# Performance work log

Measured on AMD Instinct MI355X. Metric: run time of the kernel, lower is better.

## Reference

```python
import jax, jax.numpy as jnp
import numpy as np

DM, H, B, SQ, SK = 512, 8, 8, 1024, 1024


def setup_inputs() -> dict:
    key = jax.random.key(0)
    ks = jax.random.split(key, 9)
    s = 0.02
    return {
        "Q": jax.random.normal(ks[0], (B, SQ, DM), jnp.float32),
        "K": jax.random.normal(ks[1], (B, SK, DM), jnp.float32),
        "V": jax.random.normal(ks[2], (B, SK, DM), jnp.float32),
        "mask": jax.random.randint(ks[3], (B, 1, SK), 0, 2, jnp.int32),
        "Wq": jax.random.normal(ks[4], (DM, DM), jnp.float32) * s,
        "bq": jnp.zeros((DM,), jnp.float32),
        "Wk": jax.random.normal(ks[5], (DM, DM), jnp.float32) * s,
        "bk": jnp.zeros((DM,), jnp.float32),
        "Wv": jax.random.normal(ks[6], (DM, DM), jnp.float32) * s,
        "bv": jnp.zeros((DM,), jnp.float32),
        "Wl": jax.random.normal(ks[7], (H * DM, DM), jnp.float32) * s,
        "bl": jnp.zeros((DM,), jnp.float32),
    }


def reference(Q, K, V, mask, Wq, bq, Wk, bk, Wv, bv, Wl, bl):
    # NB: the original loops h times with the SAME dense layers on full dm,
    # so all 'heads' are identical; compute once and replicate (same math).
    dm = Wq.shape[1]
    h = Wl.shape[0] // dm
    Ql = Q @ Wq + bq                                   # [B, Sq, dm]
    Kl = K @ Wk + bk                                   # [B, Sk, dm]
    Vl = V @ Wv + bv                                   # [B, Sk, dm]
    scale = jnp.sqrt(jnp.asarray(dm, jnp.float32))
    scores = jnp.einsum('bqd,bkd->bqk', Ql, Kl) / scale  # [B, Sq, Sk]
    scores = scores + mask.astype(scores.dtype) * (-1e9)  # mask [B,1,Sk] broadcasts
    att = jax.nn.softmax(scores, axis=-1)              # [B, Sq, Sk]
    head = jnp.einsum('bqk,bkd->bqd', att, Vl)         # [B, Sq, dm]
    multi = jnp.tile(head, (1, 1, h))                  # concat of h identical heads
    att_ws = jnp.broadcast_to(att[:, None], (att.shape[0], h) + att.shape[1:])
    Y = multi @ Wl + bl                                # [B, Sq, dm]
    return Y, att_ws
```

## Files before the change

kernel.cpp:

```cpp
#include <hip/hip_runtime.h>
#include <stdint.h>


typedef unsigned short u16;
typedef __attribute__((ext_vector_type(8))) short bf16x8;
typedef __attribute__((ext_vector_type(8))) unsigned short u16x8;
typedef __attribute__((ext_vector_type(4))) unsigned short u16x4;
typedef __attribute__((ext_vector_type(4))) float f32x4;

__device__ __forceinline__ u16 f2bf(float f) {
    union { float f; unsigned int u; } v; v.f = f;
    v.u += 0x7fffu + ((v.u >> 16) & 1u);
    return (u16)(v.u >> 16);
}
__device__ __forceinline__ float bf2f(u16 u) {
    union { unsigned int u; float f; } v; v.u = (unsigned int)u << 16;
    return v.f;
}

__device__ __forceinline__ void gld16(const u16* g, u16* l) {
#if __has_builtin(__builtin_amdgcn_global_load_lds)
    __builtin_amdgcn_global_load_lds(
        (const __attribute__((address_space(1))) void*)g,
        (__attribute__((address_space(3))) void*)l, 16, 0, 0);
#else
    *(uint4*)l = *(const uint4*)g;
#endif
}

__device__ __forceinline__ void gemm_core(
    const u16* __restrict__ Ab, const u16* __restrict__ Bb,
    int K, int lda, int ldb, int m0, int n0, int t,
    u16 (*As)[32], u16 (*Bs)[32], f32x4 acc[4][4])
{
    const int lane = t & 63;
    const int wm = ((t >> 6) & 1) * 64;
    const int wn = (t >> 7) * 64;
    const int sr = t >> 2, sc = (t & 3) * 8;
    const int fr = lane & 15, fk = (lane >> 4) * 8;

    for (int k0 = 0; k0 < K; k0 += 32) {
        const u16* ap = Ab + (long)(m0 + sr) * lda + (k0 + sc);
        const u16* bp = Bb + (long)(n0 + sr) * ldb + (k0 + sc);
        gld16(ap,             &As[sr][sc]);
        gld16(ap + 64L * lda, &As[sr + 64][sc]);
        gld16(bp,             &Bs[sr][sc]);
        gld16(bp + 64L * ldb, &Bs[sr + 64][sc]);
        __syncthreads();

        bf16x8 af[4], bfv[4];
        #pragma unroll
        for (int i = 0; i < 4; i++) af[i]  = *(const bf16x8*)&As[wm + i*16 + fr][fk];
        #pragma unroll
        for (int j = 0; j < 4; j++) bfv[j] = *(const bf16x8*)&Bs[wn + j*16 + fr][fk];
        #pragma unroll
        for (int i = 0; i < 4; i++)
            #pragma unroll
            for (int j = 0; j < 4; j++)
                acc[i][j] = __builtin_amdgcn_mfma_f32_16x16x32_bf16(af[i], bfv[j], acc[i][j], 0, 0, 0);
        __syncthreads();
    }
}

__device__ __forceinline__ void gemm_epilogue(
    int mode, void* Cv, const float* bias, const int* maskp,
    float scale, int ldc, int m0, int n0, int t, f32x4 acc[4][4])
{
    const int lane = t & 63;
    const int wm = ((t >> 6) & 1) * 64;
    const int wn = (t >> 7) * 64;
    const int cl = lane & 15, rl = (lane >> 4) * 4;

    float badd[4];
    #pragma unroll
    for (int j = 0; j < 4; j++) {
        int col = n0 + wn + j * 16 + cl;
        float v = bias ? bias[col] : 0.f;
        if (maskp) v += (float)maskp[col] * (-1e9f);
        badd[j] = v;
    }

    if (mode == 1) {
        u16* C = (u16*)Cv;
        #pragma unroll
        for (int i = 0; i < 4; i++)
            #pragma unroll
            for (int r = 0; r < 4; r++) {
                long row = m0 + wm + i * 16 + rl + r;
                #pragma unroll
                for (int j = 0; j < 4; j++)
                    C[(long)(n0 + wn + j * 16 + cl) * ldc + row] =
                        f2bf(acc[i][j][r] * scale + badd[j]);
            }
    } else if (mode == 2) {
        float* C = (float*)Cv;
        #pragma unroll
        for (int i = 0; i < 4; i++)
            #pragma unroll
            for (int r = 0; r < 4; r++) {
                float* crow = C + (long)(m0 + wm + i * 16 + rl + r) * ldc;
                #pragma unroll
                for (int j = 0; j < 4; j++)
                    crow[n0 + wn + j * 16 + cl] = acc[i][j][r] * scale + badd[j];
            }
    } else {
        u16* C = (u16*)Cv;
        #pragma unroll
        for (int i = 0; i < 4; i++)
            #pragma unroll
            for (int r = 0; r < 4; r++) {
                u16* crow = C + (long)(m0 + wm + i * 16 + rl + r) * ldc;
                #pragma unroll
                for (int j = 0; j < 4; j++)
                    crow[n0 + wn + j * 16 + cl] = f2bf(acc[i][j][r] * scale + badd[j]);
            }
    }
}

__global__ __launch_bounds__(256, 2)
void gemm_tn(const u16* __restrict__ A, const u16* __restrict__ B, void* __restrict__ Cv,
             const float* __restrict__ bias, const int* __restrict__ mask,
             int K, int lda, int ldb, int ldc,
             long sA, long sB, long sC, long sMask, float scale, int mode)
{
    __shared__ __align__(16) u16 As[128][32];
    __shared__ __align__(16) u16 Bs[128][32];
    const int bz = blockIdx.z;
    const int m0 = blockIdx.x * 128, n0 = blockIdx.y * 128;
    const int t = threadIdx.x;

    f32x4 acc[4][4];
    #pragma unroll
    for (int i = 0; i < 4; i++)
        #pragma unroll
        for (int j = 0; j < 4; j++) acc[i][j] = (f32x4){0.f, 0.f, 0.f, 0.f};

    gemm_core(A + (long)bz * sA, B + (long)bz * sB, K, lda, ldb, m0, n0, t, As, Bs, acc);

    void* Cb = (mode == 2) ? (void*)((float*)Cv + (long)bz * sC)
                           : (void*)((u16*)Cv + (long)bz * sC);
    const int* maskp = mask ? mask + (long)bz * sMask : nullptr;
    gemm_epilogue(mode, Cb, bias, maskp, scale, ldc, m0, n0, t, acc);
}

__global__ __launch_bounds__(256, 2)
void gemm_qkvv(const u16* __restrict__ Qb, const u16* __restrict__ Kb,
               const u16* __restrict__ Vb, const u16* __restrict__ Wqt,
               const u16* __restrict__ Wkt, const u16* __restrict__ Wct,
               u16* __restrict__ Qlb, u16* __restrict__ Klb, u16* __restrict__ Vwt,
               const float* __restrict__ bq, const float* __restrict__ bk,
               const float* __restrict__ bvs)
{
    __shared__ __align__(16) u16 As[128][32];
    __shared__ __align__(16) u16 Bs[128][32];
    const int z = blockIdx.z, seg = z >> 3, b = z & 7;
    const int m0 = blockIdx.x * 128, n0 = blockIdx.y * 128;
    const int t = threadIdx.x;
    const long sQ = 524288L;

    const u16* A; const u16* B; u16* C; const float* bias; int ldc, mode;
    if (seg == 0)      { A = Qb + b * sQ; B = Wqt; C = Qlb + b * sQ; bias = bq;  ldc = 512;  mode = 0; }
    else if (seg == 1) { A = Kb + b * sQ; B = Wkt; C = Klb + b * sQ; bias = bk;  ldc = 512;  mode = 0; }
    else               { A = Vb + b * sQ; B = Wct; C = Vwt + b * sQ; bias = bvs; ldc = 1024; mode = 1; }

    f32x4 acc[4][4];
    #pragma unroll
    for (int i = 0; i < 4; i++)
        #pragma unroll
        for (int j = 0; j < 4; j++) acc[i][j] = (f32x4){0.f, 0.f, 0.f, 0.f};

    gemm_core(A, B, 512, 512, 512, m0, n0, t, As, Bs, acc);
    gemm_epilogue(mode, C, bias, nullptr, 1.f, ldc, m0, n0, t, acc);
}

__global__ __launch_bounds__(256)
void prep_w(const float* __restrict__ Wq, const float* __restrict__ Wk,
            const float* __restrict__ Wv, const float* __restrict__ Wl,
            const float* __restrict__ bv,
            u16* __restrict__ Wqt, u16* __restrict__ Wkt,
            u16* __restrict__ Wvb, u16* __restrict__ Wst, float* __restrict__ bvs)
{
    const int bx = blockIdx.x;
    if (bx >= 4096) {
        int n = (bx - 4096) * 256 + threadIdx.x;
        if (n < 512) {
            float acc = 0.f;
            for (int k = 0; k < 512; k++) {
                float bvk = bv[k];
                if (bvk != 0.f) {
                    float s = 0.f;
                    #pragma unroll
                    for (int h = 0; h < 8; h++) s += Wl[((long)h * 512 + k) * 512 + n];
                    acc += bvk * s;
                }
            }
            bvs[n] = acc;
        }
        return;
    }
    long id = (long)bx * 256 + threadIdx.x;
    int seg = (int)(id >> 18);
    long j = id & 262143L;
    int n = (int)(j & 511), k = (int)(j >> 9);
    if (seg == 0) {
        Wqt[(long)n * 512 + k] = f2bf(Wq[(long)k * 512 + n]);
    } else if (seg == 1) {
        Wkt[(long)n * 512 + k] = f2bf(Wk[(long)k * 512 + n]);
    } else if (seg == 2) {
        Wvb[j] = f2bf(Wv[j]);
    } else {
        float s = 0.f;
        #pragma unroll
        for (int h = 0; h < 8; h++) s += Wl[((long)h * 512 + k) * 512 + n];
        Wst[(long)n * 512 + k] = f2bf(s);
    }
}

__global__ __launch_bounds__(256, 2)
void prep_qkv_wct(const float* __restrict__ Q, const float* __restrict__ K,
                  const float* __restrict__ V, u16* __restrict__ Qb,
                  u16* __restrict__ Kb, u16* __restrict__ Vb,
                  const u16* __restrict__ Wvb, const u16* __restrict__ Wst,
                  u16* __restrict__ Wct)
{
    __shared__ __align__(16) u16 As[128][32];
    __shared__ __align__(16) u16 Bs[128][32];
    const int bx = blockIdx.x;
    if (bx < 6144) {
        long id = (long)bx * 256 + threadIdx.x;
        int seg = (int)(id >> 19);
        long e = (id & 524287L) * 8;
        const float* s = seg == 0 ? Q : (seg == 1 ? K : V);
        u16* d = seg == 0 ? Qb : (seg == 1 ? Kb : Vb);
        float4 lo = *(const float4*)(s + e);
        float4 hi = *(const float4*)(s + e + 4);
        u16x8 r;
        r[0]=f2bf(lo.x); r[1]=f2bf(lo.y); r[2]=f2bf(lo.z); r[3]=f2bf(lo.w);
        r[4]=f2bf(hi.x); r[5]=f2bf(hi.y); r[6]=f2bf(hi.z); r[7]=f2bf(hi.w);
        *(u16x8*)(d + e) = r;
        return;
    }
    const int bid = bx - 6144;
    const int m0 = (bid & 3) * 128, n0 = (bid >> 2) * 128;
    const int t = threadIdx.x;
    f32x4 acc[4][4];
    #pragma unroll
    for (int i = 0; i < 4; i++)
        #pragma unroll
        for (int j = 0; j < 4; j++) acc[i][j] = (f32x4){0.f, 0.f, 0.f, 0.f};
    gemm_core(Wvb, Wst, 512, 512, 512, m0, n0, t, As, Bs, acc);
    gemm_epilogue(1, Wct, nullptr, nullptr, 1.f, 512, m0, n0, t, acc);
}

__global__ __launch_bounds__(256)
void softmax_rep(const u16* __restrict__ Sb, float* __restrict__ att,
                 u16* __restrict__ attb)
{
    const int q = blockIdx.x, b = blockIdx.y;
    const int t = threadIdx.x;
    const u16* row = Sb + ((long)b * 1024 + q) * 1024;

    u16x4 xv = *(const u16x4*)(row + t * 4);
    float x[4] = { bf2f(xv[0]), bf2f(xv[1]), bf2f(xv[2]), bf2f(xv[3]) };

    float m = fmaxf(fmaxf(x[0], x[1]), fmaxf(x[2], x[3]));
    #pragma unroll
    for (int o = 32; o > 0; o >>= 1) m = fmaxf(m, __shfl_xor(m, o));
    __shared__ float red[4];
    const int w = t >> 6;
    if ((t & 63) == 0) red[w] = m;
    __syncthreads();
    m = fmaxf(fmaxf(red[0], red[1]), fmaxf(red[2], red[3]));
    __syncthreads();

    float e[4], s = 0.f;
    #pragma unroll
    for (int i = 0; i < 4; i++) { e[i] = __expf(x[i] - m); s += e[i]; }
    #pragma unroll
    for (int o = 32; o > 0; o >>= 1) s += __shfl_xor(s, o);
    if ((t & 63) == 0) red[w] = s;
    __syncthreads();
    s = red[0] + red[1] + red[2] + red[3];
    float inv = 1.f / s;

    float a0 = e[0]*inv, a1 = e[1]*inv, a2 = e[2]*inv, a3 = e[3]*inv;
    float4 ov = make_float4(a0, a1, a2, a3);
    #pragma unroll
    for (int h = 0; h < 8; h++)
        *(float4*)(att + (((long)b * 8 + h) * 1024 + q) * 1024 + t * 4) = ov;
    u16x4 bo; bo[0]=f2bf(a0); bo[1]=f2bf(a1); bo[2]=f2bf(a2); bo[3]=f2bf(a3);
    *(u16x4*)(attb + ((long)b * 1024 + q) * 1024 + t * 4) = bo;
}

extern "C" void kernel_launch(void* const* d_in, const int* in_sizes, int n_in,
                              void* d_out, int out_size, void* d_ws, size_t ws_size,
                              hipStream_t stream)
{
    (void)in_sizes; (void)n_in; (void)out_size; (void)ws_size;

    const float* Q    = (const float*)d_in[0];
    const float* Kin  = (const float*)d_in[1];
    const float* V    = (const float*)d_in[2];
    const int*   mask = (const int*)d_in[3];
    const float* Wq   = (const float*)d_in[4];
    const float* bq   = (const float*)d_in[5];
    const float* Wk   = (const float*)d_in[6];
    const float* bk   = (const float*)d_in[7];
    const float* Wv   = (const float*)d_in[8];
    const float* bv   = (const float*)d_in[9];
    const float* Wl   = (const float*)d_in[10];
    const float* bl   = (const float*)d_in[11];

    float* out  = (float*)d_out;
    float* Yout = out;
    float* att  = out + 4194304L;

    u16*   w    = (u16*)d_ws;
    float* bvs  = (float*)w;
    u16*   Qb   = w + 1024;
    u16*   Kb   = Qb + 4194304L;
    u16*   Vb   = Kb + 4194304L;
    u16*   Wqt  = Vb + 4194304L;
    u16*   Wkt  = Wqt + 262144L;
    u16*   Wvb  = Wkt + 262144L;
    u16*   Wst  = Wvb + 262144L;
    u16*   Wct  = Wst + 262144L;
    u16*   Qlb  = Wct + 262144L;
    u16*   Klb  = Qlb + 4194304L;
    u16*   Vwt  = Klb + 4194304L;
    u16*   Sb   = Vwt + 4194304L;
    u16*   attb = Sb + 8388608L;

    const long sQ  = 524288L;
    const long sAt = 1048576L;
    const float isc = 0.04419417382415922f;

    prep_w<<<dim3(4098), dim3(256), 0, stream>>>(Wq, Wk, Wv, Wl, bv,
                                                 Wqt, Wkt, Wvb, Wst, bvs);

    prep_qkv_wct<<<dim3(6160), dim3(256), 0, stream>>>(Q, Kin, V, Qb, Kb, Vb,
                                                       Wvb, Wst, Wct);

    gemm_qkvv<<<dim3(8, 4, 24), dim3(256), 0, stream>>>(
        Qb, Kb, Vb, Wqt, Wkt, Wct, Qlb, Klb, Vwt, bq, bk, bvs);

    gemm_tn<<<dim3(8, 8, 8), dim3(256), 0, stream>>>(
        Qlb, Klb, Sb, nullptr, mask, 512, 512, 512, 1024,
        sQ, sQ, sAt, 1024L, isc, 0);

    softmax_rep<<<dim3(1024, 8), dim3(256), 0, stream>>>(Sb, att, attb);

    gemm_tn<<<dim3(8, 4, 8), dim3(256), 0, stream>>>(
        attb, Vwt, Yout, bl, nullptr, 1024, 1024, 1024, 512,
        sAt, sQ, sQ, 0L, 1.f, 2);
}
```

Measured before the change: 469.5 us.

## Fuse QK^T, masked softmax, and PV GEMM into single attention kernel

Replaces the score GEMM, standalone softmax and output GEMM with one kernel. Each block handles 16 query rows over the full 1024-key range, keeping scores in registers and the bf16 probabilities in LDS for the PV product. This removes the bf16 score and probability round-trips through global memory and two kernel launches. In exchange, K and V operands are read directly from global memory without LDS tiling, with heavy redundant reloading across only 512 blocks. Register pressure is also high.

```diff
diff --git a/kernel.cpp b/kernel.cpp
--- a/kernel.cpp
+++ b/kernel.cpp
@@ -12,10 +12,6 @@
     union { float f; unsigned int u; } v; v.f = f;
     v.u += 0x7fffu + ((v.u >> 16) & 1u);
     return (u16)(v.u >> 16);
-}
-__device__ __forceinline__ float bf2f(u16 u) {
-    union { unsigned int u; float f; } v; v.u = (unsigned int)u << 16;
-    return v.f;
 }
 
 __device__ __forceinline__ void gld16(const u16* g, u16* l) {
@@ -63,7 +59,7 @@
 }
 
 __device__ __forceinline__ void gemm_epilogue(
-    int mode, void* Cv, const float* bias, const int* maskp,
+    int mode, void* Cv, const float* bias,
     float scale, int ldc, int m0, int n0, int t, f32x4 acc[4][4])
 {
     const int lane = t & 63;
@@ -75,9 +71,7 @@
     #pragma unroll
     for (int j = 0; j < 4; j++) {
         int col = n0 + wn + j * 16 + cl;
-        float v = bias ? bias[col] : 0.f;
-        if (maskp) v += (float)maskp[col] * (-1e9f);
-        badd[j] = v;
+        badd[j] = bias ? bias[col] : 0.f;
     }
 
     if (mode == 1) {
@@ -92,17 +86,6 @@
                     C[(long)(n0 + wn + j * 16 + cl) * ldc + row] =
                         f2bf(acc[i][j][r] * scale + badd[j]);
             }
-    } else if (mode == 2) {
-        float* C = (float*)Cv;
-        #pragma unroll
-        for (int i = 0; i < 4; i++)
-            #pragma unroll
-            for (int r = 0; r < 4; r++) {
-                float* crow = C + (long)(m0 + wm + i * 16 + rl + r) * ldc;
-                #pragma unroll
-                for (int j = 0; j < 4; j++)
-                    crow[n0 + wn + j * 16 + cl] = acc[i][j][r] * scale + badd[j];
-            }
     } else {
         u16* C = (u16*)Cv;
         #pragma unroll
@@ -118,32 +101,6 @@
 }
 
 __global__ __launch_bounds__(256, 2)
-void gemm_tn(const u16* __restrict__ A, const u16* __restrict__ B, void* __restrict__ Cv,
-             const float* __restrict__ bias, const int* __restrict__ mask,
-             int K, int lda, int ldb, int ldc,
-             long sA, long sB, long sC, long sMask, float scale, int mode)
-{
-    __shared__ __align__(16) u16 As[128][32];
-    __shared__ __align__(16) u16 Bs[128][32];
-    const int bz = blockIdx.z;
-    const int m0 = blockIdx.x * 128, n0 = blockIdx.y * 128;
-    const int t = threadIdx.x;
-
-    f32x4 acc[4][4];
-    #pragma unroll
-    for (int i = 0; i < 4; i++)
-        #pragma unroll
-        for (int j = 0; j < 4; j++) acc[i][j] = (f32x4){0.f, 0.f, 0.f, 0.f};
-
-    gemm_core(A + (long)bz * sA, B + (long)bz * sB, K, lda, ldb, m0, n0, t, As, Bs, acc);
-
-    void* Cb = (mode == 2) ? (void*)((float*)Cv + (long)bz * sC)
-                           : (void*)((u16*)Cv + (long)bz * sC);
-    const int* maskp = mask ? mask + (long)bz * sMask : nullptr;
-    gemm_epilogue(mode, Cb, bias, maskp, scale, ldc, m0, n0, t, acc);
-}
-
-__global__ __launch_bounds__(256, 2)
 void gemm_qkvv(const u16* __restrict__ Qb, const u16* __restrict__ Kb,
                const u16* __restrict__ Vb, const u16* __restrict__ Wqt,
                const u16* __restrict__ Wkt, const u16* __restrict__ Wct,
@@ -170,7 +127,7 @@
         for (int j = 0; j < 4; j++) acc[i][j] = (f32x4){0.f, 0.f, 0.f, 0.f};
 
     gemm_core(A, B, 512, 512, 512, m0, n0, t, As, Bs, acc);
-    gemm_epilogue(mode, C, bias, nullptr, 1.f, ldc, m0, n0, t, acc);
+    gemm_epilogue(mode, C, bias, 1.f, ldc, m0, n0, t, acc);
 }
 
 __global__ __launch_bounds__(256)
@@ -249,47 +206,150 @@
         #pragma unroll
         for (int j = 0; j < 4; j++) acc[i][j] = (f32x4){0.f, 0.f, 0.f, 0.f};
     gemm_core(Wvb, Wst, 512, 512, 512, m0, n0, t, As, Bs, acc);
-    gemm_epilogue(1, Wct, nullptr, nullptr, 1.f, 512, m0, n0, t, acc);
-}
-
-__global__ __launch_bounds__(256)
-void softmax_rep(const u16* __restrict__ Sb, float* __restrict__ att,
-                 u16* __restrict__ attb)
-{
-    const int q = blockIdx.x, b = blockIdx.y;
-    const int t = threadIdx.x;
-    const u16* row = Sb + ((long)b * 1024 + q) * 1024;
-
-    u16x4 xv = *(const u16x4*)(row + t * 4);
-    float x[4] = { bf2f(xv[0]), bf2f(xv[1]), bf2f(xv[2]), bf2f(xv[3]) };
-
-    float m = fmaxf(fmaxf(x[0], x[1]), fmaxf(x[2], x[3]));
-    #pragma unroll
-    for (int o = 32; o > 0; o >>= 1) m = fmaxf(m, __shfl_xor(m, o));
-    __shared__ float red[4];
-    const int w = t >> 6;
-    if ((t & 63) == 0) red[w] = m;
+    gemm_epilogue(1, Wct, nullptr, 1.f, 512, m0, n0, t, acc);
+}
+
+__global__ __launch_bounds__(256, 2)
+void fused_attn(const u16* __restrict__ Qlb, const u16* __restrict__ Klb,
+                const u16* __restrict__ Vwt, const int* __restrict__ mask,
+                const float* __restrict__ bl,
+                float* __restrict__ att, float* __restrict__ Yout)
+{
+    __shared__ u16 S[16][1032];
+    __shared__ float redm[4][16];
+    __shared__ float reds[4][16];
+
+    const int r0 = blockIdx.x * 16;
+    const int b  = blockIdx.y;
+    const int t  = threadIdx.x;
+    const int w  = t >> 6, lane = t & 63;
+    const int cl = lane & 15, q4 = lane >> 4;
+    const int rl = q4 * 4;
+    const int wkv = w * 256;
+    const int wn  = w * 128;
+    const float isc = 0.04419417382415922f;
+
+    const u16* Qb = Qlb + (long)b * 524288;
+    const u16* Kb = Klb + (long)b * 524288;
+    const u16* Vb = Vwt + (long)b * 524288;
+
+    bf16x8 af[16];
+    #pragma unroll
+    for (int ks = 0; ks < 16; ks++)
+        af[ks] = *(const bf16x8*)(Qb + (long)(r0 + cl) * 512 + ks * 32 + q4 * 8);
+
+    float mf[16];
+    #pragma unroll
+    for (int j = 0; j < 16; j++)
+        mf[j] = (float)mask[b * 1024 + wkv + j * 16 + cl] * (-1e9f);
+
+    f32x4 acc[16];
+    #pragma unroll
+    for (int j = 0; j < 16; j++) acc[j] = (f32x4){0.f, 0.f, 0.f, 0.f};
+
+    #pragma unroll
+    for (int ks = 0; ks < 16; ks++) {
+        #pragma unroll
+        for (int j = 0; j < 16; j++) {
+            bf16x8 bf = *(const bf16x8*)(Kb + (long)(wkv + j * 16 + cl) * 512 + ks * 32 + q4 * 8);
+            acc[j] = __builtin_amdgcn_mfma_f32_16x16x32_bf16(af[ks], bf, acc[j], 0, 0, 0);
+        }
+    }
+
+    #pragma unroll
+    for (int j = 0; j < 16; j++)
+        #pragma unroll
+        for (int r = 0; r < 4; r++)
+            acc[j][r] = acc[j][r] * isc + mf[j];
+
+    float m[4];
+    #pragma unroll
+    for (int r = 0; r < 4; r++) {
+        float v = acc[0][r];
+        #pragma unroll
+        for (int j = 1; j < 16; j++) v = fmaxf(v, acc[j][r]);
+        #pragma unroll
+        for (int o = 1; o < 16; o <<= 1) v = fmaxf(v, __shfl_xor(v, o));
+        m[r] = v;
+    }
+    if (cl == 0) {
+        #pragma unroll
+        for (int r = 0; r < 4; r++) redm[w][rl + r] = m[r];
+    }
     __syncthreads();
-    m = fmaxf(fmaxf(red[0], red[1]), fmaxf(red[2], red[3]));
+    #pragma unroll
+    for (int r = 0; r < 4; r++)
+        m[r] = fmaxf(fmaxf(redm[0][rl + r], redm[1][rl + r]),
+                     fmaxf(redm[2][rl + r], redm[3][rl + r]));
+
+    float sm[4] = {0.f, 0.f, 0.f, 0.f};
+    #pragma unroll
+    for (int j = 0; j < 16; j++)
+        #pragma unroll
+        for (int r = 0; r < 4; r++) {
+            float e = __expf(acc[j][r] - m[r]);
+            acc[j][r] = e;
+            sm[r] += e;
+        }
+    #pragma unroll
+    for (int r = 0; r < 4; r++)
+        #pragma unroll
+        for (int o = 1; o < 16; o <<= 1) sm[r] += __shfl_xor(sm[r], o);
+    if (cl == 0) {
+        #pragma unroll
+        for (int r = 0; r < 4; r++) reds[w][rl + r] = sm[r];
+    }
     __syncthreads();
-
-    float e[4], s = 0.f;
-    #pragma unroll
-    for (int i = 0; i < 4; i++) { e[i] = __expf(x[i] - m); s += e[i]; }
-    #pragma unroll
-    for (int o = 32; o > 0; o >>= 1) s += __shfl_xor(s, o);
-    if ((t & 63) == 0) red[w] = s;
+    float inv[4];
+    #pragma unroll
+    for (int r = 0; r < 4; r++)
+        inv[r] = 1.f / (reds[0][rl + r] + reds[1][rl + r] + reds[2][rl + r] + reds[3][rl + r]);
+
+    #pragma unroll
+    for (int j = 0; j < 16; j++)
+        #pragma unroll
+        for (int r = 0; r < 4; r++) {
+            float a = acc[j][r] * inv[r];
+            acc[j][r] = a;
+            S[rl + r][wkv + j * 16 + cl] = f2bf(a);
+        }
     __syncthreads();
-    s = red[0] + red[1] + red[2] + red[3];
-    float inv = 1.f / s;
-
-    float a0 = e[0]*inv, a1 = e[1]*inv, a2 = e[2]*inv, a3 = e[3]*inv;
-    float4 ov = make_float4(a0, a1, a2, a3);
-    #pragma unroll
-    for (int h = 0; h < 8; h++)
-        *(float4*)(att + (((long)b * 8 + h) * 1024 + q) * 1024 + t * 4) = ov;
-    u16x4 bo; bo[0]=f2bf(a0); bo[1]=f2bf(a1); bo[2]=f2bf(a2); bo[3]=f2bf(a3);
-    *(u16x4*)(attb + ((long)b * 1024 + q) * 1024 + t * 4) = bo;
+
+    #pragma unroll
+    for (int r = 0; r < 4; r++) {
+        long base_r = (((long)b * 8) * 1024 + (r0 + rl + r)) * 1024 + wkv + cl;
+        #pragma unroll
+        for (int h = 0; h < 8; h++) {
+            float* p = att + base_r + (long)h * 1048576;
+            #pragma unroll
+            for (int j = 0; j < 16; j++) p[j * 16] = acc[j][r];
+        }
+    }
+
+    f32x4 acc2[8];
+    #pragma unroll
+    for (int j = 0; j < 8; j++) acc2[j] = (f32x4){0.f, 0.f, 0.f, 0.f};
+
+    #pragma unroll
+    for (int ks = 0; ks < 32; ks++) {
+        bf16x8 afv = *(const bf16x8*)&S[cl][ks * 32 + q4 * 8];
+        #pragma unroll
+        for (int j = 0; j < 8; j++) {
+            bf16x8 bf = *(const bf16x8*)(Vb + (long)(wn + j * 16 + cl) * 1024 + ks * 32 + q4 * 8);
+            acc2[j] = __builtin_amdgcn_mfma_f32_16x16x32_bf16(afv, bf, acc2[j], 0, 0, 0);
+        }
+    }
+
+    float blv[8];
+    #pragma unroll
+    for (int j = 0; j < 8; j++) blv[j] = bl[wn + j * 16 + cl];
+    #pragma unroll
+    for (int r = 0; r < 4; r++) {
+        float* yrow = Yout + (long)b * 524288 + (long)(r0 + rl + r) * 512;
+        #pragma unroll
+        for (int j = 0; j < 8; j++)
+            yrow[wn + j * 16 + cl] = acc2[j][r] + blv[j];
+    }
 }
 
 extern "C" void kernel_launch(void* const* d_in, const int* in_sizes, int n_in,
@@ -328,12 +388,6 @@
     u16*   Qlb  = Wct + 262144L;
     u16*   Klb  = Qlb + 4194304L;
     u16*   Vwt  = Klb + 4194304L;
-    u16*   Sb   = Vwt + 4194304L;
-    u16*   attb = Sb + 8388608L;
-
-    const long sQ  = 524288L;
-    const long sAt = 1048576L;
-    const float isc = 0.04419417382415922f;
 
     prep_w<<<dim3(4098), dim3(256), 0, stream>>>(Wq, Wk, Wv, Wl, bv,
                                                  Wqt, Wkt, Wvb, Wst, bvs);
@@ -344,13 +398,6 @@
     gemm_qkvv<<<dim3(8, 4, 24), dim3(256), 0, stream>>>(
         Qb, Kb, Vb, Wqt, Wkt, Wct, Qlb, Klb, Vwt, bq, bk, bvs);
 
-    gemm_tn<<<dim3(8, 8, 8), dim3(256), 0, stream>>>(
-        Qlb, Klb, Sb, nullptr, mask, 512, 512, 512, 1024,
-        sQ, sQ, sAt, 1024L, isc, 0);
-
-    softmax_rep<<<dim3(1024, 8), dim3(256), 0, stream>>>(Sb, att, attb);
-
-    gemm_tn<<<dim3(8, 4, 8), dim3(256), 0, stream>>>(
-        attb, Vwt, Yout, bl, nullptr, 1024, 1024, 1024, 512,
-        sAt, sQ, sQ, 0L, 1.f, 2);
-}
+    fused_attn<<<dim3(64, 8), dim3(256), 0, stream>>>(
+        Qlb, Klb, Vwt, mask, bl, att, Yout);
+}
```

Measured after the change: 578.8 us. 23.3% more time.

## Fold Wq·Wkᵀ into one weight to drop the K projection GEMM

Applied to the files above, without the earlier changes.

Scores are rewritten as Q(WqWkᵀ)Kᵀ plus rank-one bias terms. A precomputed Wqk product is applied to Q only, and raw K feeds the score GEMM directly. Per-row u and per-column v bias vectors are added in the score epilogue. This removes one of the three batched projection GEMMs at the cost of a small weight GEMM and two matrix-vector passes, and it may change bf16 rounding behaviour.

```diff
diff --git a/kernel.cpp b/kernel.cpp
--- a/kernel.cpp
+++ b/kernel.cpp
@@ -64,6 +64,7 @@
 
 __device__ __forceinline__ void gemm_epilogue(
     int mode, void* Cv, const float* bias, const int* maskp,
+    const float* urow, const float* vcol,
     float scale, int ldc, int m0, int n0, int t, f32x4 acc[4][4])
 {
     const int lane = t & 63;
@@ -77,6 +78,7 @@
         int col = n0 + wn + j * 16 + cl;
         float v = bias ? bias[col] : 0.f;
         if (maskp) v += (float)maskp[col] * (-1e9f);
+        if (vcol)  v += vcol[col];
         badd[j] = v;
     }
 
@@ -87,10 +89,11 @@
             #pragma unroll
             for (int r = 0; r < 4; r++) {
                 long row = m0 + wm + i * 16 + rl + r;
+                float ua = urow ? urow[row] : 0.f;
                 #pragma unroll
                 for (int j = 0; j < 4; j++)
                     C[(long)(n0 + wn + j * 16 + cl) * ldc + row] =
-                        f2bf(acc[i][j][r] * scale + badd[j]);
+                        f2bf(acc[i][j][r] * scale + badd[j] + ua);
             }
     } else if (mode == 2) {
         float* C = (float*)Cv;
@@ -98,10 +101,12 @@
         for (int i = 0; i < 4; i++)
             #pragma unroll
             for (int r = 0; r < 4; r++) {
-                float* crow = C + (long)(m0 + wm + i * 16 + rl + r) * ldc;
+                int row = m0 + wm + i * 16 + rl + r;
+                float ua = urow ? urow[row] : 0.f;
+                float* crow = C + (long)row * ldc;
                 #pragma unroll
                 for (int j = 0; j < 4; j++)
-                    crow[n0 + wn + j * 16 + cl] = acc[i][j][r] * scale + badd[j];
+                    crow[n0 + wn + j * 16 + cl] = acc[i][j][r] * scale + badd[j] + ua;
             }
     } else {
         u16* C = (u16*)Cv;
@@ -109,10 +114,12 @@
         for (int i = 0; i < 4; i++)
             #pragma unroll
             for (int r = 0; r < 4; r++) {
-                u16* crow = C + (long)(m0 + wm + i * 16 + rl + r) * ldc;
+                int row = m0 + wm + i * 16 + rl + r;
+                float ua = urow ? urow[row] : 0.f;
+                u16* crow = C + (long)row * ldc;
                 #pragma unroll
                 for (int j = 0; j < 4; j++)
-                    crow[n0 + wn + j * 16 + cl] = f2bf(acc[i][j][r] * scale + badd[j]);
+                    crow[n0 + wn + j * 16 + cl] = f2bf(acc[i][j][r] * scale + badd[j] + ua);
             }
     }
 }
@@ -120,6 +127,7 @@
 __global__ __launch_bounds__(256, 2)
 void gemm_tn(const u16* __restrict__ A, const u16* __restrict__ B, void* __restrict__ Cv,
              const float* __restrict__ bias, const int* __restrict__ mask,
+             const float* __restrict__ u, const float* __restrict__ v,
              int K, int lda, int ldb, int ldc,
              long sA, long sB, long sC, long sMask, float scale, int mode)
 {
@@ -140,16 +148,16 @@
     void* Cb = (mode == 2) ? (void*)((float*)Cv + (long)bz * sC)
                            : (void*)((u16*)Cv + (long)bz * sC);
     const int* maskp = mask ? mask + (long)bz * sMask : nullptr;
-    gemm_epilogue(mode, Cb, bias, maskp, scale, ldc, m0, n0, t, acc);
+    const float* up = u ? u + (long)bz * 1024 : nullptr;
+    const float* vp = v ? v + (long)bz * 1024 : nullptr;
+    gemm_epilogue(mode, Cb, bias, maskp, up, vp, scale, ldc, m0, n0, t, acc);
 }
 
 __global__ __launch_bounds__(256, 2)
-void gemm_qkvv(const u16* __restrict__ Qb, const u16* __restrict__ Kb,
-               const u16* __restrict__ Vb, const u16* __restrict__ Wqt,
-               const u16* __restrict__ Wkt, const u16* __restrict__ Wct,
-               u16* __restrict__ Qlb, u16* __restrict__ Klb, u16* __restrict__ Vwt,
-               const float* __restrict__ bq, const float* __restrict__ bk,
-               const float* __restrict__ bvs)
+void gemm_tv(const u16* __restrict__ Qb, const u16* __restrict__ Vb,
+             const u16* __restrict__ Wqkt, const u16* __restrict__ Wct,
+             u16* __restrict__ T1b, u16* __restrict__ Vwt,
+             const float* __restrict__ bvs)
 {
     __shared__ __align__(16) u16 As[128][32];
     __shared__ __align__(16) u16 Bs[128][32];
@@ -158,57 +166,74 @@
     const int t = threadIdx.x;
     const long sQ = 524288L;
 
-    const u16* A; const u16* B; u16* C; const float* bias; int ldc, mode;
-    if (seg == 0)      { A = Qb + b * sQ; B = Wqt; C = Qlb + b * sQ; bias = bq;  ldc = 512;  mode = 0; }
-    else if (seg == 1) { A = Kb + b * sQ; B = Wkt; C = Klb + b * sQ; bias = bk;  ldc = 512;  mode = 0; }
-    else               { A = Vb + b * sQ; B = Wct; C = Vwt + b * sQ; bias = bvs; ldc = 1024; mode = 1; }
-
     f32x4 acc[4][4];
     #pragma unroll
     for (int i = 0; i < 4; i++)
         #pragma unroll
         for (int j = 0; j < 4; j++) acc[i][j] = (f32x4){0.f, 0.f, 0.f, 0.f};
 
-    gemm_core(A, B, 512, 512, 512, m0, n0, t, As, Bs, acc);
-    gemm_epilogue(mode, C, bias, nullptr, 1.f, ldc, m0, n0, t, acc);
+    if (seg == 0) {
+        gemm_core(Qb + b * sQ, Wqkt, 512, 512, 512, m0, n0, t, As, Bs, acc);
+        gemm_epilogue(0, T1b + b * sQ, nullptr, nullptr, nullptr, nullptr,
+                      1.f, 512, m0, n0, t, acc);
+    } else {
+        gemm_core(Vb + b * sQ, Wct, 512, 512, 512, m0, n0, t, As, Bs, acc);
+        gemm_epilogue(1, Vwt + b * sQ, bvs, nullptr, nullptr, nullptr,
+                      1.f, 1024, m0, n0, t, acc);
+    }
 }
 
 __global__ __launch_bounds__(256)
 void prep_w(const float* __restrict__ Wq, const float* __restrict__ Wk,
             const float* __restrict__ Wv, const float* __restrict__ Wl,
+            const float* __restrict__ bq, const float* __restrict__ bk,
             const float* __restrict__ bv,
-            u16* __restrict__ Wqt, u16* __restrict__ Wkt,
-            u16* __restrict__ Wvb, u16* __restrict__ Wst, float* __restrict__ bvs)
+            u16* __restrict__ Wqb, u16* __restrict__ Wkb,
+            u16* __restrict__ Wvb, u16* __restrict__ Wst,
+            float* __restrict__ bvs, float* __restrict__ wqbk,
+            float* __restrict__ wkbq, float* __restrict__ c0)
 {
     const int bx = blockIdx.x;
+    const int t  = threadIdx.x;
+    if (bx >= 4098) {
+        int i = (bx - 4098) * 256 + t;
+        float sq = 0.f, sk = 0.f;
+        for (int o = 0; o < 512; o++) {
+            sq += Wq[(long)i * 512 + o] * bk[o];
+            sk += Wk[(long)i * 512 + o] * bq[o];
+        }
+        wqbk[i] = sq;
+        wkbq[i] = sk;
+        if (bx == 4098 && t == 0) {
+            float s = 0.f;
+            for (int o = 0; o < 512; o++) s += bq[o] * bk[o];
+            c0[0] = s;
+        }
+        return;
+    }
     if (bx >= 4096) {
-        int n = (bx - 4096) * 256 + threadIdx.x;
-        if (n < 512) {
-            float acc = 0.f;
-            for (int k = 0; k < 512; k++) {
-                float bvk = bv[k];
-                if (bvk != 0.f) {
-                    float s = 0.f;
-                    #pragma unroll
-                    for (int h = 0; h < 8; h++) s += Wl[((long)h * 512 + k) * 512 + n];
-                    acc += bvk * s;
-                }
+        int n = (bx - 4096) * 256 + t;
+        float acc = 0.f;
+        for (int k = 0; k < 512; k++) {
+            float bvk = bv[k];
+            if (bvk != 0.f) {
+                float s = 0.f;
+                #pragma unroll
+                for (int h = 0; h < 8; h++) s += Wl[((long)h * 512 + k) * 512 + n];
+                acc += bvk * s;
             }
-            bvs[n] = acc;
-        }
+        }
+        bvs[n] = acc;
         return;
     }
-    long id = (long)bx * 256 + threadIdx.x;
+    long id = (long)bx * 256 + t;
     int seg = (int)(id >> 18);
     long j = id & 262143L;
-    int n = (int)(j & 511), k = (int)(j >> 9);
-    if (seg == 0) {
-        Wqt[(long)n * 512 + k] = f2bf(Wq[(long)k * 512 + n]);
-    } else if (seg == 1) {
-        Wkt[(long)n * 512 + k] = f2bf(Wk[(long)k * 512 + n]);
-    } else if (seg == 2) {
-        Wvb[j] = f2bf(Wv[j]);
-    } else {
+    if (seg == 0)      Wqb[j] = f2bf(Wq[j]);
+    else if (seg == 1) Wkb[j] = f2bf(Wk[j]);
+    else if (seg == 2) Wvb[j] = f2bf(Wv[j]);
+    else {
+        int n = (int)(j & 511), k = (int)(j >> 9);
         float s = 0.f;
         #pragma unroll
         for (int h = 0; h < 8; h++) s += Wl[((long)h * 512 + k) * 512 + n];
@@ -220,14 +245,20 @@
 void prep_qkv_wct(const float* __restrict__ Q, const float* __restrict__ K,
                   const float* __restrict__ V, u16* __restrict__ Qb,
                   u16* __restrict__ Kb, u16* __restrict__ Vb,
+                  const u16* __restrict__ Wqb, const u16* __restrict__ Wkb,
                   const u16* __restrict__ Wvb, const u16* __restrict__ Wst,
-                  u16* __restrict__ Wct)
+                  u16* __restrict__ Wqkt, u16* __restrict__ Wct,
+                  const float* __restrict__ wqbk, const float* __restrict__ wkbq,
+                  const float* __restrict__ c0,
+                  float* __restrict__ u, float* __restrict__ v)
 {
     __shared__ __align__(16) u16 As[128][32];
     __shared__ __align__(16) u16 Bs[128][32];
     const int bx = blockIdx.x;
+    const int t  = threadIdx.x;
+
     if (bx < 6144) {
-        long id = (long)bx * 256 + threadIdx.x;
+        long id = (long)bx * 256 + t;
         int seg = (int)(id >> 19);
         long e = (id & 524287L) * 8;
         const float* s = seg == 0 ? Q : (seg == 1 ? K : V);
@@ -240,16 +271,59 @@
         *(u16x8*)(d + e) = r;
         return;
     }
-    const int bid = bx - 6144;
-    const int m0 = (bid & 3) * 128, n0 = (bid >> 2) * 128;
-    const int t = threadIdx.x;
-    f32x4 acc[4][4];
-    #pragma unroll
-    for (int i = 0; i < 4; i++)
-        #pragma unroll
-        for (int j = 0; j < 4; j++) acc[i][j] = (f32x4){0.f, 0.f, 0.f, 0.f};
-    gemm_core(Wvb, Wst, 512, 512, 512, m0, n0, t, As, Bs, acc);
-    gemm_epilogue(1, Wct, nullptr, nullptr, 1.f, 512, m0, n0, t, acc);
+    if (bx < 6176) {
+        const int bid = bx - 6144;
+        const int which = bid >> 4;
+        const int sub = bid & 15;
+        const int m0 = (sub & 3) * 128, n0 = (sub >> 2) * 128;
+        f32x4 acc[4][4];
+        #pragma unroll
+        for (int i = 0; i < 4; i++)
+            #pragma unroll
+            for (int j = 0; j < 4; j++) acc[i][j] = (f32x4){0.f, 0.f, 0.f, 0.f};
+        if (which == 0) {
+            gemm_core(Wqb, Wkb, 512, 512, 512, m0, n0, t, As, Bs, acc);
+            gemm_epilogue(1, Wqkt, nullptr, nullptr, nullptr, nullptr,
+                          1.f, 512, m0, n0, t, acc);
+        } else {
+            gemm_core(Wvb, Wst, 512, 512, 512, m0, n0, t, As, Bs, acc);
+            gemm_epilogue(1, Wct, nullptr, nullptr, nullptr, nullptr,
+                          1.f, 512, m0, n0, t, acc);
+        }
+        return;
+    }
+    {
+        const int bid = bx - 6176;
+        const int isv = bid >> 4;
+        const int sub = bid & 15;
+        const float* src = isv ? K : Q;
+        const float* wvp = isv ? wkbq : wqbk;
+        float* dst = isv ? v : u;
+        const float cadd = isv ? 0.f : c0[0];
+
+        __shared__ float wsh[512];
+        wsh[t] = wvp[t];
+        wsh[t + 256] = wvp[t + 256];
+        __syncthreads();
+
+        const int w = t >> 6, lane = t & 63;
+        float wc0, wc1, wc2, wc3, wc4, wc5, wc6, wc7;
+        {
+            const float* p = &wsh[lane * 8];
+            wc0=p[0]; wc1=p[1]; wc2=p[2]; wc3=p[3]; wc4=p[4]; wc5=p[5]; wc6=p[6]; wc7=p[7];
+        }
+        for (int r = 0; r < 128; r++) {
+            long row = (long)sub * 512 + w * 128 + r;
+            const float* p = src + row * 512 + lane * 8;
+            float4 a = *(const float4*)p;
+            float4 b2 = *(const float4*)(p + 4);
+            float s = a.x*wc0 + a.y*wc1 + a.z*wc2 + a.w*wc3
+                    + b2.x*wc4 + b2.y*wc5 + b2.z*wc6 + b2.w*wc7;
+            #pragma unroll
+            for (int o = 1; o < 64; o <<= 1) s += __shfl_xor(s, o);
+            if (lane == 0) dst[row] = s + cadd;
+        }
+    }
 }
 
 __global__ __launch_bounds__(256)
@@ -317,17 +391,22 @@
 
     u16*   w    = (u16*)d_ws;
     float* bvs  = (float*)w;
-    u16*   Qb   = w + 1024;
+    float* wqbk = bvs + 512;
+    float* wkbq = wqbk + 512;
+    float* c0   = wkbq + 512;
+    float* uvec = c0 + 512;
+    float* vvec = uvec + 8192;
+    u16*   Qb   = w + 2L * (512*4 + 8192*2);
     u16*   Kb   = Qb + 4194304L;
     u16*   Vb   = Kb + 4194304L;
-    u16*   Wqt  = Vb + 4194304L;
-    u16*   Wkt  = Wqt + 262144L;
-    u16*   Wvb  = Wkt + 262144L;
+    u16*   Wqb  = Vb + 4194304L;
+    u16*   Wkb  = Wqb + 262144L;
+    u16*   Wvb  = Wkb + 262144L;
     u16*   Wst  = Wvb + 262144L;
-    u16*   Wct  = Wst + 262144L;
-    u16*   Qlb  = Wct + 262144L;
-    u16*   Klb  = Qlb + 4194304L;
-    u16*   Vwt  = Klb + 4194304L;
+    u16*   Wqkt = Wst + 262144L;
+    u16*   Wct  = Wqkt + 262144L;
+    u16*   T1b  = Wct + 262144L;
+    u16*   Vwt  = T1b + 4194304L;
     u16*   Sb   = Vwt + 4194304L;
     u16*   attb = Sb + 8388608L;
 
@@ -335,22 +414,23 @@
     const long sAt = 1048576L;
     const float isc = 0.04419417382415922f;
 
-    prep_w<<<dim3(4098), dim3(256), 0, stream>>>(Wq, Wk, Wv, Wl, bv,
-                                                 Wqt, Wkt, Wvb, Wst, bvs);
-
-    prep_qkv_wct<<<dim3(6160), dim3(256), 0, stream>>>(Q, Kin, V, Qb, Kb, Vb,
-                                                       Wvb, Wst, Wct);
-
-    gemm_qkvv<<<dim3(8, 4, 24), dim3(256), 0, stream>>>(
-        Qb, Kb, Vb, Wqt, Wkt, Wct, Qlb, Klb, Vwt, bq, bk, bvs);
+    prep_w<<<dim3(4100), dim3(256), 0, stream>>>(
+        Wq, Wk, Wv, Wl, bq, bk, bv, Wqb, Wkb, Wvb, Wst, bvs, wqbk, wkbq, c0);
+
+    prep_qkv_wct<<<dim3(6208), dim3(256), 0, stream>>>(
+        Q, Kin, V, Qb, Kb, Vb, Wqb, Wkb, Wvb, Wst, Wqkt, Wct,
+        wqbk, wkbq, c0, uvec, vvec);
+
+    gemm_tv<<<dim3(8, 4, 16), dim3(256), 0, stream>>>(
+        Qb, Vb, Wqkt, Wct, T1b, Vwt, bvs);
 
     gemm_tn<<<dim3(8, 8, 8), dim3(256), 0, stream>>>(
-        Qlb, Klb, Sb, nullptr, mask, 512, 512, 512, 1024,
+        T1b, Kb, Sb, nullptr, mask, uvec, vvec, 512, 512, 512, 1024,
         sQ, sQ, sAt, 1024L, isc, 0);
 
     softmax_rep<<<dim3(1024, 8), dim3(256), 0, stream>>>(Sb, att, attb);
 
     gemm_tn<<<dim3(8, 4, 8), dim3(256), 0, stream>>>(
-        attb, Vwt, Yout, bl, nullptr, 1024, 1024, 1024, 512,
+        attb, Vwt, Yout, bl, nullptr, nullptr, nullptr, 1024, 1024, 1024, 512,
         sAt, sQ, sQ, 0L, 1.f, 2);
 }
```

New measurement: 516.4 us. 10.0% more time.
